# Kernel tuning notes

Hardware: AMD Instinct MI355X
Metric: run time of the kernel (lower is better)

## Reference

```python
import jax, jax.numpy as jnp
import numpy as np

N_NODES = 20000
N_EDGES = 320000
F_IN = 512
HID = 64
N_GRAPHS = 64
N_CLASSES = 5
SLOPE = 0.2      # PyG GATConv default negative_slope
EPS_BN = 1e-5


def setup_inputs() -> dict:
    key = jax.random.key(0)
    k = jax.random.split(key, 16)
    s = 0.05
    rn = lambda kk, sh: jax.random.normal(kk, sh, jnp.float32) * s
    return {
        "x": jax.random.normal(k[0], (N_NODES, F_IN), jnp.float32),
        "edge_index": jax.random.randint(k[1], (2, N_EDGES), 0, N_NODES, jnp.int32),
        "batch": jnp.sort(jax.random.randint(k[2], (N_NODES,), 0, N_GRAPHS, jnp.int32)),
        "W1": rn(k[3], (F_IN, 4 * HID)),
        "a1_src": rn(k[4], (4, HID)), "a1_dst": rn(k[5], (4, HID)),
        "b1": jnp.zeros((4 * HID,), jnp.float32),
        "bn1_gamma": jnp.ones((4 * HID,), jnp.float32), "bn1_beta": jnp.zeros((4 * HID,), jnp.float32),
        "bn1_mean": jnp.zeros((4 * HID,), jnp.float32), "bn1_var": jnp.ones((4 * HID,), jnp.float32),
        "W2": rn(k[6], (4 * HID, 4 * HID)),
        "a2_src": rn(k[7], (4, HID)), "a2_dst": rn(k[8], (4, HID)),
        "b2": jnp.zeros((4 * HID,), jnp.float32),
        "bn2_gamma": jnp.ones((4 * HID,), jnp.float32), "bn2_beta": jnp.zeros((4 * HID,), jnp.float32),
        "bn2_mean": jnp.zeros((4 * HID,), jnp.float32), "bn2_var": jnp.ones((4 * HID,), jnp.float32),
        "W3": rn(k[9], (4 * HID, HID)),
        "a3_src": rn(k[10], (1, HID)), "a3_dst": rn(k[11], (1, HID)),
        "b3": jnp.zeros((HID,), jnp.float32),
        "lin1_w": rn(k[12], (HID, HID // 2)), "lin1_b": jnp.zeros((HID // 2,), jnp.float32),
        "lin2_w": rn(k[13], (HID // 2, N_CLASSES)), "lin2_b": jnp.zeros((N_CLASSES,), jnp.float32),
    }


def _gat(x, src, dst, W, a_s, a_d, b, heads, concat):
    """PyG-style GATConv (eval mode, self-loops already in src/dst)."""
    n = x.shape[0]
    h = (x @ W).reshape(n, heads, -1)                         # [N,H,C]
    al_s = (h * a_s).sum(-1)                                  # [N,H]
    al_d = (h * a_d).sum(-1)                                  # [N,H]
    e = jax.nn.leaky_relu(al_s[src] + al_d[dst], SLOPE)       # [E,H]
    m = jax.lax.stop_gradient(jax.ops.segment_max(e, dst, num_segments=n))
    ee = jnp.exp(e - m[dst])
    denom = jax.ops.segment_sum(ee, dst, num_segments=n)      # [N,H]
    alpha = ee / (denom[dst] + 1e-16)                         # segment softmax over dst
    out = jax.ops.segment_sum(h[src] * alpha[:, :, None], dst, num_segments=n)  # [N,H,C]
    out = out.reshape(n, -1) if concat else out.mean(axis=1)
    return out + b


def _bn(x, g, b, m, v):  # BatchNorm1d, eval mode
    return (x - m) * jax.lax.rsqrt(v + EPS_BN) * g + b


def reference(x, edge_index, batch, W1, a1_src, a1_dst, b1, bn1_gamma, bn1_beta, bn1_mean, bn1_var, W2, a2_src, a2_dst, b2, bn2_gamma, bn2_beta, bn2_mean, bn2_var, W3, a3_src, a3_dst, b3, lin1_w, lin1_b, lin2_w, lin2_b):
    n = x.shape[0]
    loops = jnp.arange(n, dtype=edge_index.dtype)             # GATConv add_self_loops=True
    src = jnp.concatenate([edge_index[0], loops])
    dst = jnp.concatenate([edge_index[1], loops])
    h = _gat(x, src, dst, W1, a1_src, a1_dst, b1, 4, True)
    h = jax.nn.relu(_bn(h, bn1_gamma, bn1_beta, bn1_mean, bn1_var))
    h = _gat(h, src, dst, W2, a2_src, a2_dst, b2, 4, True)
    h = jax.nn.relu(_bn(h, bn2_gamma, bn2_beta, bn2_mean, bn2_var))
    h = jax.nn.relu(_gat(h, src, dst, W3, a3_src, a3_dst, b3, 1, False))
    sums = jax.ops.segment_sum(h, batch, num_segments=N_GRAPHS)
    cnt = jax.ops.segment_sum(jnp.ones((n, 1), h.dtype), batch, num_segments=N_GRAPHS)
    g = sums / jnp.maximum(cnt, 1.0)                          # global_mean_pool
    g = jax.nn.relu(g @ lin1_w + lin1_b)
    return g @ lin2_w + lin2_b
```

## Files before the change

kernel.cpp:

```cpp
#include <hip/hip_runtime.h>

#define N_NODES 20000
#define N_EDGES 320000
#define E_TOT   340000
#define N_GRAPHS 64
#define N_CLASSES 5
#define SLOPE 0.2f
#define EPS_BN 1e-5f

typedef _Float16 v8h __attribute__((ext_vector_type(8)));
typedef float v4f __attribute__((ext_vector_type(4)));
typedef _Float16 v4h __attribute__((ext_vector_type(4)));

#define SPQ (N_NODES * 512 / 4)
#define W1E (512 * 256)
#define W2E (256 * 256)
#define W3E (256 * 64)
#define ALZ (80000 * 4 + 20000 * 2)

__global__ __launch_bounds__(256) void k_prep(const float* __restrict__ x,
                                              _Float16* __restrict__ xh,
                                              const float* __restrict__ W1, _Float16* __restrict__ bt1,
                                              const float* __restrict__ W2, _Float16* __restrict__ bt2,
                                              const float* __restrict__ W3, _Float16* __restrict__ bt3,
                                              const int* __restrict__ batch, int* __restrict__ gstart,
                                              int* __restrict__ cnt, float* __restrict__ sums,
                                              float* __restrict__ albase) {
    int id = blockIdx.x * 256 + threadIdx.x;
    if (id < SPQ) {
        const float4 v = *(const float4*)(x + (size_t)id * 4);
        v4h h;
        h.x = (_Float16)v.x; h.y = (_Float16)v.y; h.z = (_Float16)v.z; h.w = (_Float16)v.w;
        *(v4h*)(xh + (size_t)id * 4) = h;
        return;
    }
    id -= SPQ;
    if (id < W1E) {
        const int K = 512, N = 256;
        int n = id / K, k = id - n * K;
        bt1[id] = (_Float16)W1[(size_t)k * N + n];
        return;
    }
    id -= W1E;
    if (id < W2E) {
        const int K = 256, N = 256;
        int n = id / K, k = id - n * K;
        bt2[id] = (_Float16)W2[(size_t)k * N + n];
        return;
    }
    id -= W2E;
    if (id < W3E) {
        const int K = 256, N = 64;
        int n = id / K, k = id - n * K;
        bt3[id] = (_Float16)W3[(size_t)k * N + n];
        return;
    }
    id -= W3E;
    if (id < N_NODES) {
        int i = id;
        int b = batch[i];
        if (i == 0) {
            for (int g = 0; g <= b; ++g) gstart[g] = 0;
        } else {
            int p = batch[i - 1];
            for (int g = p + 1; g <= b; ++g) gstart[g] = i;
        }
        if (i == N_NODES - 1) {
            for (int g = b + 1; g <= N_GRAPHS; ++g) gstart[g] = N_NODES;
        }
        return;
    }
    id -= N_NODES;
    if (id < N_NODES) { cnt[id] = 0; return; }
    id -= N_NODES;
    if (id < N_GRAPHS * 64) { sums[id] = 0.f; return; }
    id -= N_GRAPHS * 64;
    if (id < ALZ) albase[id] = 0.f;
}

__global__ void k_count(const int* __restrict__ ei, int* __restrict__ cnt) {
    int e = blockIdx.x * 256 + threadIdx.x;
    if (e >= E_TOT) return;
    int d = (e < N_EDGES) ? ei[N_EDGES + e] : (e - N_EDGES);
    atomicAdd(&cnt[d], 1);
}

__global__ __launch_bounds__(1024) void k_scan(const int* __restrict__ cnt,
                                               int* __restrict__ indptr,
                                               int* __restrict__ wptr) {
    __shared__ int smem[1024];
    const int t = threadIdx.x;
    const int per = (N_NODES + 1023) / 1024;
    const int i0 = t * per;
    int lsum = 0;
    for (int j = 0; j < per; ++j) {
        int i = i0 + j;
        if (i < N_NODES) lsum += cnt[i];
    }
    smem[t] = lsum;
    __syncthreads();
    for (int off = 1; off < 1024; off <<= 1) {
        int v = (t >= off) ? smem[t - off] : 0;
        __syncthreads();
        smem[t] += v;
        __syncthreads();
    }
    int run = smem[t] - lsum;
    for (int j = 0; j < per; ++j) {
        int i = i0 + j;
        if (i < N_NODES) {
            indptr[i] = run;
            wptr[i] = run;
            run += cnt[i];
        }
    }
    if (t == 1023) indptr[N_NODES] = E_TOT;
}

__global__ void k_scatter(const int* __restrict__ ei, int* __restrict__ wptr,
                          int* __restrict__ esrc) {
    int e = blockIdx.x * 256 + threadIdx.x;
    if (e >= E_TOT) return;
    int s, d;
    if (e < N_EDGES) { s = ei[e]; d = ei[N_EDGES + e]; }
    else             { s = d = e - N_EDGES; }
    int pos = atomicAdd(&wptr[d], 1);
    esrc[pos] = s;
}

template <int TN, int KK>
__global__ __launch_bounds__(256) void k_gemm_mfma(const _Float16* __restrict__ A,
                                                   const _Float16* __restrict__ Bt,
                                                   _Float16* __restrict__ H,
                                                   const float* __restrict__ aw_s,
                                                   const float* __restrict__ aw_d,
                                                   float* __restrict__ als,
                                                   float* __restrict__ ald,
                                                   int HS,
                                                   int M, int N) {
    constexpr int NTB = 2 * TN;
    constexpr int NFRAG = 2 * NTB * 64;
    constexpr int NITER = NFRAG / 256;
    constexpr int LDSW = NFRAG * 8 + (NFRAG >> 4) * 8;
    __shared__ _Float16 lbh[LDSW];
    const int tid = threadIdx.x;
    const int wave = tid >> 6, lane = tid & 63;
    const int wr = wave >> 1, wc = wave & 1;
    const int q = lane >> 4, r = lane & 15;
    const int m0 = blockIdx.x * 64 + wr * 32;
    const int n0 = blockIdx.y * (NTB * 16);
    size_t abase[2];
#pragma unroll
    for (int mi = 0; mi < 2; ++mi) {
        int ar = m0 + mi * 16 + r;
        if (ar >= M) ar = M - 1;
        abase[mi] = (size_t)ar * KK + q * 8;
    }
    size_t gaddr[NITER];
    int loff[NITER];
#pragma unroll
    for (int j = 0; j < NITER; ++j) {
        const int f = tid + j * 256;
        const int qq = f & 3;
        const int ss = (f >> 2) & 1;
        const int rr = (f >> 3) & 15;
        const int tt = f >> 7;
        gaddr[j] = (size_t)(n0 + tt * 16 + rr) * KK + ss * 32 + qq * 8;
        const int fi = (ss * NTB + tt) * 64 + qq * 16 + rr;
        loff[j] = fi * 8 + (fi >> 4) * 8;
    }
    v4f acc[2][TN];
#pragma unroll
    for (int mi = 0; mi < 2; ++mi)
#pragma unroll
        for (int t = 0; t < TN; ++t) acc[mi][t] = (v4f){0.f, 0.f, 0.f, 0.f};

    v8h ch[NITER];
#pragma unroll
    for (int j = 0; j < NITER; ++j) ch[j] = *(const v8h*)(Bt + gaddr[j]);

#pragma unroll
    for (int kc = 0; kc < KK; kc += 64) {
        __syncthreads();
#pragma unroll
        for (int j = 0; j < NITER; ++j) *(v8h*)&lbh[loff[j]] = ch[j];
        __syncthreads();
        if (kc + 64 < KK) {
#pragma unroll
            for (int j = 0; j < NITER; ++j) ch[j] = *(const v8h*)(Bt + gaddr[j] + kc + 64);
        }
#pragma unroll
        for (int ss = 0; ss < 2; ++ss) {
            v8h ah[2];
#pragma unroll
            for (int mi = 0; mi < 2; ++mi)
                ah[mi] = *(const v8h*)(A + abase[mi] + kc + ss * 32);
#pragma unroll
            for (int t = 0; t < TN; ++t) {
                const int fib = (ss * NTB + wc * TN + t) * 4 + q;
                const int off = (fib * 16 + r) * 8 + fib * 8;
                const v8h bh = *(const v8h*)&lbh[off];
#pragma unroll
                for (int mi = 0; mi < 2; ++mi)
                    acc[mi][t] = __builtin_amdgcn_mfma_f32_16x16x32_f16(ah[mi], bh, acc[mi][t], 0, 0, 0);
            }
        }
    }
#pragma unroll
    for (int mi = 0; mi < 2; ++mi)
#pragma unroll
        for (int t = 0; t < TN; ++t)
#pragma unroll
            for (int i = 0; i < 4; ++i) {
                const int row = m0 + mi * 16 + q * 4 + i;
                if (row < M) H[(size_t)row * N + n0 + (wc * TN + t) * 16 + r] = (_Float16)acc[mi][t][i];
            }
    const int colbase = n0 + wc * TN * 16;
    const int hd = colbase >> 6;
#pragma unroll
    for (int mi = 0; mi < 2; ++mi)
#pragma unroll
        for (int i = 0; i < 4; ++i) {
            float sp = 0.f, dp = 0.f;
#pragma unroll
            for (int t = 0; t < TN; ++t) {
                const int col = colbase + t * 16 + r;
                sp += acc[mi][t][i] * aw_s[col];
                dp += acc[mi][t][i] * aw_d[col];
            }
#pragma unroll
            for (int m = 1; m < 16; m <<= 1) {
                sp += __shfl_xor(sp, m, 64);
                dp += __shfl_xor(dp, m, 64);
            }
            const int row = m0 + mi * 16 + q * 4 + i;
            if (r == 0 && row < M) {
                atomicAdd(&als[row * HS + hd], sp);
                atomicAdd(&ald[row * HS + hd], dp);
            }
        }
}

__global__ __launch_bounds__(256) void k_agg4(const _Float16* __restrict__ hin,
                                              const float* __restrict__ als,
                                              const float* __restrict__ ald,
                                              const int* __restrict__ indptr,
                                              const int* __restrict__ esrc,
                                              const float* __restrict__ bias,
                                              const float* __restrict__ gamma,
                                              const float* __restrict__ beta,
                                              const float* __restrict__ mean,
                                              const float* __restrict__ var,
                                              _Float16* __restrict__ pho) {
    __shared__ float lacc[2][64][4];
    __shared__ float lsm[2][64];
    const int pair = threadIdx.x >> 7;
    const int wv   = (threadIdx.x >> 6) & 1;
    const int lane = threadIdx.x & 63;
    const int n = blockIdx.x * 2 + pair;
    const int beg = indptr[n], end = indptr[n + 1];
    const int mid = beg + ((end - beg + 1) >> 1);
    const int e0 = wv ? mid : beg;
    const int e1 = wv ? end : mid;
    const int head = lane >> 4;
    const float aldn = ald[n * 4 + head];
    float4 acc = {0.f, 0.f, 0.f, 0.f};
    float sm = 0.f;
    const int c = lane * 4;
    int e = e0;
    for (; e + 3 < e1; e += 4) {
        const int s0 = esrc[e], s1 = esrc[e + 1], s2 = esrc[e + 2], s3 = esrc[e + 3];
        float v0 = als[s0 * 4 + head] + aldn;
        float v1 = als[s1 * 4 + head] + aldn;
        float v2 = als[s2 * 4 + head] + aldn;
        float v3 = als[s3 * 4 + head] + aldn;
        const v4h h0 = *(const v4h*)(hin + (size_t)s0 * 256 + c);
        const v4h h1 = *(const v4h*)(hin + (size_t)s1 * 256 + c);
        const v4h h2 = *(const v4h*)(hin + (size_t)s2 * 256 + c);
        const v4h h3 = *(const v4h*)(hin + (size_t)s3 * 256 + c);
        v0 = (v0 > 0.f) ? v0 : SLOPE * v0;
        v1 = (v1 > 0.f) ? v1 : SLOPE * v1;
        v2 = (v2 > 0.f) ? v2 : SLOPE * v2;
        v3 = (v3 > 0.f) ? v3 : SLOPE * v3;
        const float a0 = __expf(v0), a1 = __expf(v1), a2 = __expf(v2), a3 = __expf(v3);
        sm += (a0 + a1) + (a2 + a3);
        acc.x += a0 * (float)h0.x + a1 * (float)h1.x + a2 * (float)h2.x + a3 * (float)h3.x;
        acc.y += a0 * (float)h0.y + a1 * (float)h1.y + a2 * (float)h2.y + a3 * (float)h3.y;
        acc.z += a0 * (float)h0.z + a1 * (float)h1.z + a2 * (float)h2.z + a3 * (float)h3.z;
        acc.w += a0 * (float)h0.w + a1 * (float)h1.w + a2 * (float)h2.w + a3 * (float)h3.w;
    }
    for (; e < e1; ++e) {
        const int s0 = esrc[e];
        float v0 = als[s0 * 4 + head] + aldn;
        const v4h h0 = *(const v4h*)(hin + (size_t)s0 * 256 + c);
        v0 = (v0 > 0.f) ? v0 : SLOPE * v0;
        const float a0 = __expf(v0);
        sm += a0;
        acc.x += a0 * (float)h0.x; acc.y += a0 * (float)h0.y;
        acc.z += a0 * (float)h0.z; acc.w += a0 * (float)h0.w;
    }
    if (wv == 1) {
        lacc[pair][lane][0] = acc.x; lacc[pair][lane][1] = acc.y;
        lacc[pair][lane][2] = acc.z; lacc[pair][lane][3] = acc.w;
        lsm[pair][lane] = sm;
    }
    __syncthreads();
    if (wv == 0) {
        acc.x += lacc[pair][lane][0]; acc.y += lacc[pair][lane][1];
        acc.z += lacc[pair][lane][2]; acc.w += lacc[pair][lane][3];
        sm += lsm[pair][lane];
        const float invd = 1.f / (sm + 1e-16f);
        float y[4] = {acc.x * invd, acc.y * invd, acc.z * invd, acc.w * invd};
        v4h oh;
#pragma unroll
        for (int i = 0; i < 4; ++i) {
            float t = y[i] + bias[c + i];
            t = (t - mean[c + i]) * rsqrtf(var[c + i] + EPS_BN) * gamma[c + i] + beta[c + i];
            t = fmaxf(t, 0.f);
            oh[i] = (_Float16)t;
        }
        *(v4h*)(pho + (size_t)n * 256 + c) = oh;
    }
}

__global__ __launch_bounds__(256) void k_agg1(const _Float16* __restrict__ hin,
                                              const float* __restrict__ als,
                                              const float* __restrict__ ald,
                                              const int* __restrict__ indptr,
                                              const int* __restrict__ esrc,
                                              const float* __restrict__ bias,
                                              const int* __restrict__ batch,
                                              float* __restrict__ sums) {
    const int n = blockIdx.x * 4 + (threadIdx.x >> 6);
    const int lane = threadIdx.x & 63;
    const int beg = indptr[n], end = indptr[n + 1];
    const float aldn = ald[n];
    float acc = 0.f, sm = 0.f;
    int e = beg;
    for (; e + 3 < end; e += 4) {
        const int s0 = esrc[e], s1 = esrc[e + 1], s2 = esrc[e + 2], s3 = esrc[e + 3];
        float v0 = als[s0] + aldn;
        float v1 = als[s1] + aldn;
        float v2 = als[s2] + aldn;
        float v3 = als[s3] + aldn;
        const float h0 = (float)hin[(size_t)s0 * 64 + lane];
        const float h1 = (float)hin[(size_t)s1 * 64 + lane];
        const float h2 = (float)hin[(size_t)s2 * 64 + lane];
        const float h3 = (float)hin[(size_t)s3 * 64 + lane];
        v0 = (v0 > 0.f) ? v0 : SLOPE * v0;
        v1 = (v1 > 0.f) ? v1 : SLOPE * v1;
        v2 = (v2 > 0.f) ? v2 : SLOPE * v2;
        v3 = (v3 > 0.f) ? v3 : SLOPE * v3;
        const float a0 = __expf(v0), a1 = __expf(v1), a2 = __expf(v2), a3 = __expf(v3);
        sm += (a0 + a1) + (a2 + a3);
        acc += a0 * h0 + a1 * h1 + a2 * h2 + a3 * h3;
    }
    for (; e < end; ++e) {
        const int s0 = esrc[e];
        float v0 = als[s0] + aldn;
        const float h0 = (float)hin[(size_t)s0 * 64 + lane];
        v0 = (v0 > 0.f) ? v0 : SLOPE * v0;
        const float a0 = __expf(v0);
        sm += a0;
        acc += a0 * h0;
    }
    const float invd = 1.f / (sm + 1e-16f);
    const float val = fmaxf(acc * invd + bias[lane], 0.f);
    atomicAdd(&sums[batch[n] * 64 + lane], val);
}

__global__ void k_mlp(const float* __restrict__ sums, const int* __restrict__ gstart,
                      const float* __restrict__ w1, const float* __restrict__ b1,
                      const float* __restrict__ w2, const float* __restrict__ b2,
                      float* __restrict__ outp) {
    const int g = blockIdx.x;
    const int t = threadIdx.x;
    __shared__ float hid[32];
    const int cntn = gstart[g + 1] - gstart[g];
    const float inv = 1.f / (float)max(cntn, 1);
    float acc = b1[t];
    for (int c = 0; c < 64; ++c) acc += (sums[g * 64 + c] * inv) * w1[c * 32 + t];
    hid[t] = fmaxf(acc, 0.f);
    __syncthreads();
    if (t < N_CLASSES) {
        float o = b2[t];
        for (int k = 0; k < 32; ++k) o += hid[k] * w2[k * 5 + t];
        outp[g * 5 + t] = o;
    }
}

extern "C" void kernel_launch(void* const* d_in, const int* in_sizes, int n_in,
                              void* d_out, int out_size, void* d_ws, size_t ws_size,
                              hipStream_t stream) {
    const float* x        = (const float*)d_in[0];
    const int* edge_index = (const int*)d_in[1];
    const int* batch      = (const int*)d_in[2];
    const float* W1  = (const float*)d_in[3];
    const float* a1s = (const float*)d_in[4];
    const float* a1d = (const float*)d_in[5];
    const float* b1  = (const float*)d_in[6];
    const float* g1  = (const float*)d_in[7];
    const float* be1 = (const float*)d_in[8];
    const float* mu1 = (const float*)d_in[9];
    const float* va1 = (const float*)d_in[10];
    const float* W2  = (const float*)d_in[11];
    const float* a2s = (const float*)d_in[12];
    const float* a2d = (const float*)d_in[13];
    const float* b2  = (const float*)d_in[14];
    const float* g2  = (const float*)d_in[15];
    const float* be2 = (const float*)d_in[16];
    const float* mu2 = (const float*)d_in[17];
    const float* va2 = (const float*)d_in[18];
    const float* W3  = (const float*)d_in[19];
    const float* a3s = (const float*)d_in[20];
    const float* a3d = (const float*)d_in[21];
    const float* b3  = (const float*)d_in[22];
    const float* l1w = (const float*)d_in[23];
    const float* l1b = (const float*)d_in[24];
    const float* l2w = (const float*)d_in[25];
    const float* l2b = (const float*)d_in[26];
    float* out = (float*)d_out;

    char* w = (char*)d_ws;
    size_t off = 0;
    auto alloc = [&](size_t bytes) -> void* {
        void* p = w + off;
        off += (bytes + 255) & ~(size_t)255;
        return p;
    };
    _Float16* xh   = (_Float16*)alloc((size_t)N_NODES * 512 * 2);
    _Float16* phf  = xh;
    _Float16* bufH  = (_Float16*)alloc((size_t)N_NODES * 256 * 2);
    _Float16* bufH3 = (_Float16*)alloc((size_t)N_NODES * 64 * 2);
    _Float16* bt1 = (_Float16*)alloc((size_t)512 * 256 * 2);
    _Float16* bt2 = (_Float16*)alloc((size_t)256 * 256 * 2);
    _Float16* bt3 = (_Float16*)alloc((size_t)256 * 64 * 2);
    float* albase = (float*)alloc((size_t)ALZ * 4);
    float* als1 = albase;
    float* ald1 = albase + 80000;
    float* als2 = albase + 160000;
    float* ald2 = albase + 240000;
    float* als3 = albase + 320000;
    float* ald3 = albase + 340000;
    int* cnt      = (int*)alloc((size_t)N_NODES * 4);
    int* wptr     = (int*)alloc((size_t)N_NODES * 4);
    int* indptr   = (int*)alloc((size_t)(N_NODES + 1) * 4);
    int* esrc     = (int*)alloc((size_t)E_TOT * 4);
    int* gstart   = (int*)alloc((size_t)(N_GRAPHS + 1) * 4);
    float* sums   = (float*)alloc((size_t)N_GRAPHS * 64 * 4);

    const int PREP_IDS = SPQ + W1E + W2E + W3E + N_NODES + N_NODES + N_GRAPHS * 64 + ALZ;
    k_prep<<<(PREP_IDS + 255) / 256, 256, 0, stream>>>(x, xh, W1, bt1, W2, bt2, W3, bt3,
                                                       batch, gstart, cnt, sums, albase);
    k_count<<<(E_TOT + 255) / 256, 256, 0, stream>>>(edge_index, cnt);
    k_scan<<<1, 1024, 0, stream>>>(cnt, indptr, wptr);
    k_scatter<<<(E_TOT + 255) / 256, 256, 0, stream>>>(edge_index, wptr, esrc);

    const int MB = (N_NODES + 63) / 64;

    k_gemm_mfma<4, 512><<<dim3(MB, 2), 256, 0, stream>>>(xh, bt1, bufH,
                                                         a1s, a1d, als1, ald1, 4,
                                                         N_NODES, 256);
    k_agg4<<<N_NODES / 2, 256, 0, stream>>>(bufH, als1, ald1, indptr, esrc, b1, g1, be1, mu1, va1, phf);
    k_gemm_mfma<4, 256><<<dim3(MB, 2), 256, 0, stream>>>(phf, bt2, bufH,
                                                         a2s, a2d, als2, ald2, 4,
                                                         N_NODES, 256);
    k_agg4<<<N_NODES / 2, 256, 0, stream>>>(bufH, als2, ald2, indptr, esrc, b2, g2, be2, mu2, va2, phf);
    k_gemm_mfma<2, 256><<<dim3(MB, 1), 256, 0, stream>>>(phf, bt3, bufH3,
                                                         a3s, a3d, als3, ald3, 1,
                                                         N_NODES, 64);
    k_agg1<<<N_NODES / 4, 256, 0, stream>>>(bufH3, als3, ald3, indptr, esrc, b3, batch, sums);
    k_mlp<<<N_GRAPHS, 32, 0, stream>>>(sums, gstart, l1w, l1b, l2w, l2b, out);
}
```

Measured before the change: 351.2 us.

## Fuse CSR build into persistent blocks overlapped with first-layer GEMM

Replaces the separate count, single-block scan and scatter kernels with a 96-block device-side CSR build using custom grid barriers. That build runs inside one launch alongside the layer-1 MFMA GEMM tiles, so graph construction overlaps the GEMM. The aim is to remove three kernel launches and the serial single-block scan, and to hide CSR work behind the GEMM. The cost is spin-wait barriers that deadlock unless all 96 CSR blocks are co-resident, plus an extra memset of the control words.

```diff
diff --git a/kernel.cpp b/kernel.cpp
--- a/kernel.cpp
+++ b/kernel.cpp
@@ -8,6 +8,9 @@
 #define SLOPE 0.2f
 #define EPS_BN 1e-5f
 
+#define CB 96
+#define NCH 209
+
 typedef _Float16 v8h __attribute__((ext_vector_type(8)));
 typedef float v4f __attribute__((ext_vector_type(4)));
 typedef _Float16 v4h __attribute__((ext_vector_type(4)));
@@ -17,6 +20,10 @@
 #define W2E (256 * 256)
 #define W3E (256 * 64)
 #define ALZ (80000 * 4 + 20000 * 2)
+#define PREP_IDS (SPQ + W1E + W2E + W3E + N_NODES + N_NODES + N_GRAPHS * 64 + ALZ)
+
+#define RELBASE 384
+#define CTRL_INTS (RELBASE + 3 * 256)
 
 __global__ __launch_bounds__(256) void k_prep(const float* __restrict__ x,
                                               _Float16* __restrict__ xh,
@@ -78,82 +85,98 @@
     if (id < ALZ) albase[id] = 0.f;
 }
 
-__global__ void k_count(const int* __restrict__ ei, int* __restrict__ cnt) {
-    int e = blockIdx.x * 256 + threadIdx.x;
-    if (e >= E_TOT) return;
-    int d = (e < N_EDGES) ? ei[N_EDGES + e] : (e - N_EDGES);
-    atomicAdd(&cnt[d], 1);
-}
-
-__global__ __launch_bounds__(1024) void k_scan(const int* __restrict__ cnt,
-                                               int* __restrict__ indptr,
-                                               int* __restrict__ wptr) {
-    __shared__ int smem[1024];
-    const int t = threadIdx.x;
-    const int per = (N_NODES + 1023) / 1024;
-    const int i0 = t * per;
-    int lsum = 0;
-    for (int j = 0; j < per; ++j) {
-        int i = i0 + j;
-        if (i < N_NODES) lsum += cnt[i];
-    }
-    smem[t] = lsum;
+__device__ __forceinline__ void gsync96(int* ctrl, int k, int bid) {
+    int* arr = ctrl + k * CB;
+    int* rel = ctrl + RELBASE + k * 256;
     __syncthreads();
-    for (int off = 1; off < 1024; off <<= 1) {
-        int v = (t >= off) ? smem[t - off] : 0;
+    if (threadIdx.x == 0) {
+        __builtin_amdgcn_fence(__ATOMIC_RELEASE, "agent");
+        __hip_atomic_store(&arr[bid], 1, __ATOMIC_RELAXED, __HIP_MEMORY_SCOPE_AGENT);
+    }
+    if (bid == 0) {
+        if ((int)threadIdx.x < CB) {
+            while (__hip_atomic_load(&arr[threadIdx.x], __ATOMIC_RELAXED, __HIP_MEMORY_SCOPE_AGENT) == 0)
+                __builtin_amdgcn_s_sleep(8);
+        }
         __syncthreads();
-        smem[t] += v;
+        if (threadIdx.x < 8) {
+            __hip_atomic_store(&rel[threadIdx.x * 32], 1, __ATOMIC_RELAXED, __HIP_MEMORY_SCOPE_AGENT);
+        }
+        if (threadIdx.x == 0)
+            __builtin_amdgcn_fence(__ATOMIC_ACQUIRE, "agent");
+    } else if (threadIdx.x == 0) {
+        int* myrel = &rel[(bid & 7) * 32];
+        while (__hip_atomic_load(myrel, __ATOMIC_RELAXED, __HIP_MEMORY_SCOPE_AGENT) == 0)
+            __builtin_amdgcn_s_sleep(8);
+        __builtin_amdgcn_fence(__ATOMIC_ACQUIRE, "agent");
+    }
+    __syncthreads();
+}
+
+__device__ void csr_build(const int* __restrict__ ei, int* __restrict__ cnt,
+                          int* __restrict__ wptr, int* __restrict__ indptr,
+                          int* __restrict__ esrc, int* __restrict__ blocksum,
+                          int* __restrict__ ctrl, int bid, int tid, int* ssc) {
+    for (int e = bid * 256 + tid; e < E_TOT; e += CB * 256) {
+        int d = (e < N_EDGES) ? ei[N_EDGES + e] : (e - N_EDGES);
+        atomicAdd(&cnt[d], 1);
+    }
+    gsync96(ctrl, 0, bid);
+    const int i = bid * NCH + tid;
+    const int active = (tid < NCH && i < N_NODES);
+    int ls = active ? cnt[i] : 0;
+    ssc[tid] = ls;
+    __syncthreads();
+    for (int off = 1; off < 256; off <<= 1) {
+        int v = (tid >= off) ? ssc[tid - off] : 0;
         __syncthreads();
-    }
-    int run = smem[t] - lsum;
-    for (int j = 0; j < per; ++j) {
-        int i = i0 + j;
-        if (i < N_NODES) {
-            indptr[i] = run;
-            wptr[i] = run;
-            run += cnt[i];
-        }
-    }
-    if (t == 1023) indptr[N_NODES] = E_TOT;
-}
-
-__global__ void k_scatter(const int* __restrict__ ei, int* __restrict__ wptr,
-                          int* __restrict__ esrc) {
-    int e = blockIdx.x * 256 + threadIdx.x;
-    if (e >= E_TOT) return;
-    int s, d;
-    if (e < N_EDGES) { s = ei[e]; d = ei[N_EDGES + e]; }
-    else             { s = d = e - N_EDGES; }
-    int pos = atomicAdd(&wptr[d], 1);
-    esrc[pos] = s;
+        ssc[tid] += v;
+        __syncthreads();
+    }
+    const int epre = ssc[tid] - ls;
+    if (tid == 255) blocksum[bid] = ssc[255];
+    gsync96(ctrl, 1, bid);
+    int boff = 0;
+    for (int j = 0; j < bid; ++j) boff += blocksum[j];
+    if (active) {
+        const int run = boff + epre;
+        indptr[i] = run;
+        wptr[i] = run;
+    }
+    if (bid == 0 && tid == 0) indptr[N_NODES] = E_TOT;
+    gsync96(ctrl, 2, bid);
+    for (int e = bid * 256 + tid; e < E_TOT; e += CB * 256) {
+        int s, d;
+        if (e < N_EDGES) { s = ei[e]; d = ei[N_EDGES + e]; }
+        else             { s = d = e - N_EDGES; }
+        int pos = atomicAdd(&wptr[d], 1);
+        esrc[pos] = s;
+    }
 }
 
 template <int TN, int KK>
-__global__ __launch_bounds__(256) void k_gemm_mfma(const _Float16* __restrict__ A,
-                                                   const _Float16* __restrict__ Bt,
-                                                   _Float16* __restrict__ H,
-                                                   const float* __restrict__ aw_s,
-                                                   const float* __restrict__ aw_d,
-                                                   float* __restrict__ als,
-                                                   float* __restrict__ ald,
-                                                   int HS,
-                                                   int M, int N) {
+__device__ void gemm_tile(const _Float16* __restrict__ A,
+                          const _Float16* __restrict__ Bt,
+                          _Float16* __restrict__ H,
+                          const float* __restrict__ aw_s,
+                          const float* __restrict__ aw_d,
+                          float* __restrict__ als,
+                          float* __restrict__ ald,
+                          int HS, int N, int bx, int by, _Float16* lbh) {
     constexpr int NTB = 2 * TN;
     constexpr int NFRAG = 2 * NTB * 64;
     constexpr int NITER = NFRAG / 256;
-    constexpr int LDSW = NFRAG * 8 + (NFRAG >> 4) * 8;
-    __shared__ _Float16 lbh[LDSW];
     const int tid = threadIdx.x;
     const int wave = tid >> 6, lane = tid & 63;
     const int wr = wave >> 1, wc = wave & 1;
     const int q = lane >> 4, r = lane & 15;
-    const int m0 = blockIdx.x * 64 + wr * 32;
-    const int n0 = blockIdx.y * (NTB * 16);
+    const int m0 = bx * 64 + wr * 32;
+    const int n0 = by * (NTB * 16);
     size_t abase[2];
 #pragma unroll
     for (int mi = 0; mi < 2; ++mi) {
         int ar = m0 + mi * 16 + r;
-        if (ar >= M) ar = M - 1;
+        if (ar >= N_NODES) ar = N_NODES - 1;
         abase[mi] = (size_t)ar * KK + q * 8;
     }
     size_t gaddr[NITER];
@@ -213,7 +236,7 @@
 #pragma unroll
             for (int i = 0; i < 4; ++i) {
                 const int row = m0 + mi * 16 + q * 4 + i;
-                if (row < M) H[(size_t)row * N + n0 + (wc * TN + t) * 16 + r] = (_Float16)acc[mi][t][i];
+                if (row < N_NODES) H[(size_t)row * N + n0 + (wc * TN + t) * 16 + r] = (_Float16)acc[mi][t][i];
             }
     const int colbase = n0 + wc * TN * 16;
     const int hd = colbase >> 6;
@@ -234,11 +257,47 @@
                 dp += __shfl_xor(dp, m, 64);
             }
             const int row = m0 + mi * 16 + q * 4 + i;
-            if (r == 0 && row < M) {
+            if (r == 0 && row < N_NODES) {
                 atomicAdd(&als[row * HS + hd], sp);
                 atomicAdd(&ald[row * HS + hd], dp);
             }
         }
+}
+
+__global__ __launch_bounds__(256) void k_p1(const int* __restrict__ ei,
+                                            int* __restrict__ cnt, int* __restrict__ wptr,
+                                            int* __restrict__ indptr, int* __restrict__ esrc,
+                                            int* __restrict__ blocksum, int* __restrict__ ctrl,
+                                            const _Float16* __restrict__ xh,
+                                            const _Float16* __restrict__ bt1,
+                                            _Float16* __restrict__ bufH,
+                                            const float* __restrict__ a1s,
+                                            const float* __restrict__ a1d,
+                                            float* __restrict__ als1, float* __restrict__ ald1) {
+    __shared__ __align__(16) char smraw[17472];
+    const int bid = blockIdx.x;
+    const int tid = threadIdx.x;
+    if (bid < CB) {
+        csr_build(ei, cnt, wptr, indptr, esrc, blocksum, ctrl, bid, tid, (int*)smraw);
+    } else {
+        const int t = bid - CB;
+        if (t < 626) gemm_tile<4, 512>(xh, bt1, bufH, a1s, a1d, als1, ald1, 4, 256,
+                                       t >> 1, t & 1, (_Float16*)smraw);
+    }
+}
+
+template <int TN, int KK>
+__global__ __launch_bounds__(256) void k_gemm(const _Float16* __restrict__ A,
+                                              const _Float16* __restrict__ Bt,
+                                              _Float16* __restrict__ H,
+                                              const float* __restrict__ aw_s,
+                                              const float* __restrict__ aw_d,
+                                              float* __restrict__ als,
+                                              float* __restrict__ ald,
+                                              int HS, int N) {
+    __shared__ __align__(16) char smraw[17472];
+    gemm_tile<TN, KK>(A, Bt, H, aw_s, aw_d, als, ald, HS, N,
+                      blockIdx.x, blockIdx.y, (_Float16*)smraw);
 }
 
 __global__ __launch_bounds__(256) void k_agg4(const _Float16* __restrict__ hin,
@@ -448,27 +507,19 @@
     int* esrc     = (int*)alloc((size_t)E_TOT * 4);
     int* gstart   = (int*)alloc((size_t)(N_GRAPHS + 1) * 4);
     float* sums   = (float*)alloc((size_t)N_GRAPHS * 64 * 4);
-
-    const int PREP_IDS = SPQ + W1E + W2E + W3E + N_NODES + N_NODES + N_GRAPHS * 64 + ALZ;
+    int* blocksum = (int*)alloc((size_t)CB * 4);
+    int* ctrl     = (int*)alloc((size_t)CTRL_INTS * 4);
+
+    hipMemsetAsync(ctrl, 0, (size_t)CTRL_INTS * 4, stream);
+
     k_prep<<<(PREP_IDS + 255) / 256, 256, 0, stream>>>(x, xh, W1, bt1, W2, bt2, W3, bt3,
                                                        batch, gstart, cnt, sums, albase);
-    k_count<<<(E_TOT + 255) / 256, 256, 0, stream>>>(edge_index, cnt);
-    k_scan<<<1, 1024, 0, stream>>>(cnt, indptr, wptr);
-    k_scatter<<<(E_TOT + 255) / 256, 256, 0, stream>>>(edge_index, wptr, esrc);
-
-    const int MB = (N_NODES + 63) / 64;
-
-    k_gemm_mfma<4, 512><<<dim3(MB, 2), 256, 0, stream>>>(xh, bt1, bufH,
-                                                         a1s, a1d, als1, ald1, 4,
-                                                         N_NODES, 256);
+    k_p1<<<CB + 626, 256, 0, stream>>>(edge_index, cnt, wptr, indptr, esrc, blocksum, ctrl,
+                                       xh, bt1, bufH, a1s, a1d, als1, ald1);
     k_agg4<<<N_NODES / 2, 256, 0, stream>>>(bufH, als1, ald1, indptr, esrc, b1, g1, be1, mu1, va1, phf);
-    k_gemm_mfma<4, 256><<<dim3(MB, 2), 256, 0, stream>>>(phf, bt2, bufH,
-                                                         a2s, a2d, als2, ald2, 4,
-                                                         N_NODES, 256);
+    k_gemm<4, 256><<<dim3(313, 2), 256, 0, stream>>>(phf, bt2, bufH, a2s, a2d, als2, ald2, 4, 256);
     k_agg4<<<N_NODES / 2, 256, 0, stream>>>(bufH, als2, ald2, indptr, esrc, b2, g2, be2, mu2, va2, phf);
-    k_gemm_mfma<2, 256><<<dim3(MB, 1), 256, 0, stream>>>(phf, bt3, bufH3,
-                                                         a3s, a3d, als3, ald3, 1,
-                                                         N_NODES, 64);
+    k_gemm<2, 256><<<dim3(313, 1), 256, 0, stream>>>(phf, bt3, bufH3, a3s, a3d, als3, ald3, 1, 64);
     k_agg1<<<N_NODES / 4, 256, 0, stream>>>(bufH3, als3, ald3, indptr, esrc, b3, batch, sums);
     k_mlp<<<N_GRAPHS, 32, 0, stream>>>(sums, gstart, l1w, l1b, l2w, l2b, out);
 }
```

Result: faster. 311.3 us (-11.4%).
